# Kernel tuning notes

Hardware: AMD Instinct MI355X
Metric: run time of the kernel (lower is better)

## Reference

```python
import jax, jax.numpy as jnp
import numpy as np

D_IN = 1024
D_OUT = 1024

def setup_inputs() -> dict:
    key = jax.random.key(0)
    kx, kq, kk, kv = jax.random.split(key, 4)
    x = jax.random.normal(kx, (4, 4096, D_IN), dtype=jnp.float32)
    s = 1.0 / np.sqrt(D_IN)
    Wq = jax.random.uniform(kq, (D_IN, D_OUT), dtype=jnp.float32, minval=-s, maxval=s)
    Wk = jax.random.uniform(kk, (D_IN, D_OUT), dtype=jnp.float32, minval=-s, maxval=s)
    Wv = jax.random.uniform(kv, (D_IN, D_OUT), dtype=jnp.float32, minval=-s, maxval=s)
    return {"x": x, "Wq": Wq, "Wk": Wk, "Wv": Wv}

def reference(x, Wq, Wk, Wv):
    # x: [B, S, d_in]; single-head causal attention (dropout p=0 => identity)
    B, S, _ = x.shape
    Q = jnp.einsum('bsd,de->bse', x, Wq)
    K = jnp.einsum('bsd,de->bse', x, Wk)
    V = jnp.einsum('bsd,de->bse', x, Wv)
    scale = 1.0 / jnp.sqrt(jnp.asarray(K.shape[-1], dtype=Q.dtype))
    scores = jnp.einsum('bqe,bke->bqk', Q, K) * scale  # [B, S, S]
    causal = jnp.tril(jnp.ones((S, S), dtype=bool))     # mask upper triangle (diag=1)
    scores = jnp.where(causal, scores, -jnp.inf)
    weights = jax.nn.softmax(scores, axis=-1)
    return jnp.einsum('bqk,bke->bqe', weights, V)
```

## Files before the change

### kernel.cpp

```cpp
#include <hip/hip_runtime.h>
#include <hip/hip_bf16.h>
#include <stdint.h>

typedef short short8 __attribute__((ext_vector_type(8)));
typedef short short4v __attribute__((ext_vector_type(4)));
typedef float f32x4 __attribute__((ext_vector_type(4)));

static __device__ __forceinline__ short f2bf(float f) {
  union { float f; uint32_t u; } v; v.f = f;
  uint32_t r = (v.u + 0x7fffu + ((v.u >> 16) & 1u)) >> 16;
  return (short)(uint16_t)r;
}
static __device__ __forceinline__ float bf2f(short h) {
  union { uint32_t u; float f; } v; v.u = ((uint32_t)(uint16_t)h) << 16;
  return v.f;
}

#define MFMA(a, b, c) __builtin_amdgcn_mfma_f32_16x16x32_bf16((a), (b), (c), 0, 0, 0)

static __device__ __forceinline__ void gload16(const short* g, short* l) {
  __builtin_amdgcn_global_load_lds(
      (const __attribute__((address_space(1))) void*)g,
      (__attribute__((address_space(3))) void*)l, 16, 0, 0);
}

static __device__ __forceinline__ void gemm256_m201(
    const short* __restrict__ Ag, int lda,
    const short* __restrict__ Bg, int ldb, int kext,
    short* lds, int t, f32x4 (&acc)[8][4])
{
  const int w = t >> 6, lane = t & 63;
  const int lr = lane & 15, lk = lane >> 4;
  const int wm = w >> 2, wn = w & 3;
  const int nk = kext >> 6;

  short* const Ab0 = lds;
  short* const Ab1 = lds + 16384;
  short* const Bb0 = lds + 32768;
  short* const Bb1 = lds + 49152;

  const int qr = t >> 3;
  const int qc = (t & 7) ^ (qr & 7);
  const short* Asrc = Ag + (size_t)qr * lda + qc * 8;
  const short* Bsrc = Bg + (size_t)qr * ldb + qc * 8;

#define STAGE_A(tile, q) gload16(Asrc + (size_t)(q) * 64 * lda + (tile) * 64, \
    (((tile) & 1) ? Ab1 : Ab0) + (q) * 4096 + w * 512)
#define STAGE_B(tile, q) gload16(Bsrc + (size_t)(q) * 64 * ldb + (tile) * 64, \
    (((tile) & 1) ? Bb1 : Bb0) + (q) * 4096 + w * 512)

  const int chq0 = ((lk) ^ (lr & 7)) * 8;
  const int chq1 = ((4 + lk) ^ (lr & 7)) * 8;
  const int arow0 = (wm * 128 + lr) * 64;
  const int brow0 = (wn * 64 + lr) * 64;

  STAGE_B(0, 0); STAGE_B(0, 2); STAGE_B(0, 1); STAGE_B(0, 3);
  STAGE_A(0, 0); STAGE_A(0, 2); STAGE_A(0, 1); STAGE_A(0, 3);
  asm volatile("s_waitcnt vmcnt(2)" ::: "memory");
  __builtin_amdgcn_s_barrier();

  for (int tt = 0; tt < nk; ++tt) {
    const short* Ac = (tt & 1) ? Ab1 : Ab0;
    const short* Bc = (tt & 1) ? Bb1 : Bb0;
    const int nx = tt + 1;
    const bool st = nx < nk;
    short8 b0[4], b1[4], af[4];

#pragma unroll
    for (int mt = 0; mt < 4; ++mt)
      af[mt] = *(const short8*)&Ac[arow0 + mt * 1024 + chq0];
#pragma unroll
    for (int nt = 0; nt < 4; ++nt)
      b0[nt] = *(const short8*)&Bc[brow0 + nt * 1024 + chq0];
    if (st) { STAGE_B(nx, 0); STAGE_B(nx, 2); }
    __builtin_amdgcn_s_barrier();
    asm volatile("s_waitcnt lgkmcnt(0)" ::: "memory");
    __builtin_amdgcn_sched_barrier(0);
    __builtin_amdgcn_s_setprio(1);
#pragma unroll
    for (int mt = 0; mt < 4; ++mt)
#pragma unroll
      for (int nt = 0; nt < 4; ++nt)
        acc[mt][nt] = MFMA(af[mt], b0[nt], acc[mt][nt]);
    __builtin_amdgcn_s_setprio(0);
    __builtin_amdgcn_s_barrier();

#pragma unroll
    for (int mt = 0; mt < 4; ++mt)
      af[mt] = *(const short8*)&Ac[arow0 + mt * 1024 + chq1];
#pragma unroll
    for (int nt = 0; nt < 4; ++nt)
      b1[nt] = *(const short8*)&Bc[brow0 + nt * 1024 + chq1];
    if (st) { STAGE_B(nx, 1); STAGE_B(nx, 3); }
    __builtin_amdgcn_s_barrier();
    asm volatile("s_waitcnt lgkmcnt(0)" ::: "memory");
    __builtin_amdgcn_sched_barrier(0);
    __builtin_amdgcn_s_setprio(1);
#pragma unroll
    for (int mt = 0; mt < 4; ++mt)
#pragma unroll
      for (int nt = 0; nt < 4; ++nt)
        acc[mt][nt] = MFMA(af[mt], b1[nt], acc[mt][nt]);
    __builtin_amdgcn_s_setprio(0);
    if (st) { asm volatile("s_waitcnt vmcnt(4)" ::: "memory"); }
    else    { asm volatile("s_waitcnt vmcnt(0)" ::: "memory"); }
    __builtin_amdgcn_s_barrier();

#pragma unroll
    for (int mt = 0; mt < 4; ++mt)
      af[mt] = *(const short8*)&Ac[arow0 + 4096 + mt * 1024 + chq0];
    if (st) { STAGE_A(nx, 0); STAGE_A(nx, 2); }
    __builtin_amdgcn_s_barrier();
    asm volatile("s_waitcnt lgkmcnt(0)" ::: "memory");
    __builtin_amdgcn_sched_barrier(0);
    __builtin_amdgcn_s_setprio(1);
#pragma unroll
    for (int mt = 0; mt < 4; ++mt)
#pragma unroll
      for (int nt = 0; nt < 4; ++nt)
        acc[4 + mt][nt] = MFMA(af[mt], b0[nt], acc[4 + mt][nt]);
    __builtin_amdgcn_s_setprio(0);
    __builtin_amdgcn_s_barrier();

#pragma unroll
    for (int mt = 0; mt < 4; ++mt)
      af[mt] = *(const short8*)&Ac[arow0 + 4096 + mt * 1024 + chq1];
    if (st) { STAGE_A(nx, 1); STAGE_A(nx, 3); }
    __builtin_amdgcn_s_barrier();
    asm volatile("s_waitcnt lgkmcnt(0)" ::: "memory");
    __builtin_amdgcn_sched_barrier(0);
    __builtin_amdgcn_s_setprio(1);
#pragma unroll
    for (int mt = 0; mt < 4; ++mt)
#pragma unroll
      for (int nt = 0; nt < 4; ++nt)
        acc[4 + mt][nt] = MFMA(af[mt], b1[nt], acc[4 + mt][nt]);
    __builtin_amdgcn_s_setprio(0);
    if (st) { asm volatile("s_waitcnt vmcnt(2)" ::: "memory"); }
    else    { asm volatile("s_waitcnt vmcnt(0)" ::: "memory"); }
    __builtin_amdgcn_s_barrier();
  }
#undef STAGE_A
#undef STAGE_B
}

static __device__ __forceinline__ void gemm_tile128(
    const short* __restrict__ Ag, int lda,
    const short* __restrict__ Bg, int ldb, int kext,
    short* Alds, short* Blds, int w, int lane, f32x4 (&acc)[4][4])
{
  const int wr = (w >> 1) * 64, wc = (w & 1) * 64;
  const int lr = lane & 15, lk = lane >> 4;

  const int c0 = w * 128 + lane;
  const int c1 = c0 + 64;
  const int r0 = c0 >> 2, cg0 = (c0 & 3) ^ ((r0 >> 1) & 3);
  const int r1 = c1 >> 2, cg1 = (c1 & 3) ^ ((r1 >> 1) & 3);
  const short* a0 = Ag + (size_t)r0 * lda + cg0 * 8;
  const short* a1 = Ag + (size_t)r1 * lda + cg1 * 8;
  const short* b0 = Bg + (size_t)r0 * ldb + cg0 * 8;
  const short* b1 = Bg + (size_t)r1 * ldb + cg1 * 8;
  short* la0 = Alds + w * 1024;
  short* la1 = la0 + 512;
  short* lb0 = Blds + w * 1024;
  short* lb1 = lb0 + 512;

  int ra[4], rb[4];
#pragma unroll
  for (int mt = 0; mt < 4; ++mt) {
    int rl = wr + mt * 16 + lr;
    ra[mt] = rl * 32 + (lk ^ ((rl >> 1) & 3)) * 8;
  }
#pragma unroll
  for (int nt = 0; nt < 4; ++nt) {
    int rl = wc + nt * 16 + lr;
    rb[nt] = rl * 32 + (lk ^ ((rl >> 1) & 3)) * 8;
  }

  for (int kk = 0; kk < kext; kk += 32) {
    if (kk) __syncthreads();
    gload16(a0 + kk, la0);
    gload16(a1 + kk, la1);
    gload16(b0 + kk, lb0);
    gload16(b1 + kk, lb1);
    __syncthreads();
    short8 af[4], bfr[4];
#pragma unroll
    for (int mt = 0; mt < 4; ++mt) af[mt] = *(const short8*)&Alds[ra[mt]];
#pragma unroll
    for (int nt = 0; nt < 4; ++nt) bfr[nt] = *(const short8*)&Blds[rb[nt]];
#pragma unroll
    for (int mt = 0; mt < 4; ++mt)
#pragma unroll
      for (int nt = 0; nt < 4; ++nt)
        acc[mt][nt] = MFMA(af[mt], bfr[nt], acc[mt][nt]);
  }
}

__global__ __launch_bounds__(256)
void cvt_x(const float* __restrict__ x, short* __restrict__ xb) {
  size_t i = (size_t)blockIdx.x * 256 + threadIdx.x;
  f32x4 a = *(const f32x4*)(x + i * 8);
  f32x4 b = *(const f32x4*)(x + i * 8 + 4);
  short8 h = { f2bf(a.x), f2bf(a.y), f2bf(a.z), f2bf(a.w),
               f2bf(b.x), f2bf(b.y), f2bf(b.z), f2bf(b.w) };
  *(short8*)(xb + i * 8) = h;
}

__global__ __launch_bounds__(256)
void cvt_w(const float* __restrict__ Wq, const float* __restrict__ Wk,
           const float* __restrict__ Wv, short* __restrict__ wt) {
  __shared__ short Tl[128][136];
  const int z = blockIdx.z;
  const float* W = (z == 0) ? Wq : (z == 1) ? Wk : Wv;
  const float scale = (z == 0) ? 0.03125f : 1.0f;
  const int c0 = blockIdx.x * 128, r0 = blockIdx.y * 128;
  const int t = threadIdx.x;
#pragma unroll
  for (int j = 0; j < 16; ++j) {
    int id = j * 256 + t;
    int row = id >> 5, c4 = id & 31;
    f32x4 v = *(const f32x4*)(W + (size_t)(r0 + row) * 1024 + c0 + c4 * 4);
#pragma unroll
    for (int cc = 0; cc < 4; ++cc) Tl[c4 * 4 + cc][row] = f2bf(v[cc] * scale);
  }
  __syncthreads();
  short* dst = wt + (size_t)z * 1048576;
#pragma unroll
  for (int j = 0; j < 8; ++j) {
    int id = j * 256 + t;
    int col = id >> 4, r8 = id & 15;
    *(short8*)(dst + (size_t)(c0 + col) * 1024 + r0 + r8 * 8) =
        *(const short8*)&Tl[col][r8 * 8];
  }
}

__global__ __launch_bounds__(512, 2)
void qkv_gemm(const short* __restrict__ xb, const short* __restrict__ wt,
              short* __restrict__ q, short* __restrict__ k,
              short* __restrict__ vt) {
  extern __shared__ short lds[];
  const int z = blockIdx.z;
  const int n0 = blockIdx.x * 256, m0 = blockIdx.y * 256;
  const int t = threadIdx.x;
  f32x4 acc[8][4] = {};
  gemm256_m201(xb + (size_t)m0 * 1024, 1024,
               wt + (size_t)z * 1048576 + (size_t)n0 * 1024, 1024, 1024,
               lds, t, acc);
  const int w = t >> 6, lane = t & 63;
  const int lr = lane & 15, lk = lane >> 4;
  const int wm = w >> 2, wn = w & 3;
#pragma unroll
  for (int mt = 0; mt < 8; ++mt) {
#pragma unroll
    for (int nt = 0; nt < 4; ++nt) {
      int col = n0 + wn * 64 + nt * 16 + lr;
      int rbase = m0 + wm * 128 + mt * 16 + lk * 4;
      if (z == 2) {
        int bb = rbase >> 12, s = rbase & 4095;
        short4v h = { f2bf(acc[mt][nt][0]), f2bf(acc[mt][nt][1]),
                      f2bf(acc[mt][nt][2]), f2bf(acc[mt][nt][3]) };
        *(short4v*)(vt + ((size_t)bb * 1024 + col) * 4096 + s) = h;
      } else {
        short* dst = (z == 0) ? q : k;
#pragma unroll
        for (int i = 0; i < 4; ++i)
          dst[(size_t)(rbase + i) * 1024 + col] = f2bf(acc[mt][nt][i]);
      }
    }
  }
}

__global__ __launch_bounds__(512, 2)
void s_gemm(const short* __restrict__ q, const short* __restrict__ k,
            short* __restrict__ P, float* __restrict__ lpart) {
  extern __shared__ short lds[];
  const int bid = blockIdx.x;
  const int b = bid & 3, tt = bid >> 2;
  int ti = (int)((sqrtf(8.f * tt + 1.f) - 1.f) * 0.5f);
  while ((ti + 1) * (ti + 2) / 2 <= tt) ++ti;
  while (ti * (ti + 1) / 2 > tt) --ti;
  const int tj = tt - ti * (ti + 1) / 2;
  const int t = threadIdx.x;
  f32x4 acc[8][4] = {};
  gemm256_m201(q + ((size_t)(b * 4096 + ti * 256)) * 1024, 1024,
               k + ((size_t)(b * 4096 + tj * 256)) * 1024, 1024, 1024,
               lds, t, acc);
  const int w = t >> 6, lane = t & 63;
  const int lr = lane & 15, lk = lane >> 4;
  const int wm = w >> 2, wn = w & 3;
  const bool diag = (ti == tj);
#pragma unroll
  for (int mt = 0; mt < 8; ++mt) {
#pragma unroll
    for (int i = 0; i < 4; ++i) {
      const int rl = wm * 128 + mt * 16 + lk * 4 + i;
      size_t prow = ((size_t)(b * 4096 + ti * 256 + rl)) * 4096 + tj * 256;
      float rs = 0.f;
#pragma unroll
      for (int nt = 0; nt < 4; ++nt) {
        const int cl = wn * 64 + nt * 16 + lr;
        float e = (!diag || cl <= rl) ? __expf(acc[mt][nt][i]) : 0.f;
        short pb = f2bf(e);
        P[prow + cl] = pb;
        rs += bf2f(pb);
      }
      rs += __shfl_xor(rs, 1);
      rs += __shfl_xor(rs, 2);
      rs += __shfl_xor(rs, 4);
      rs += __shfl_xor(rs, 8);
      if (lr == 0)
        lpart[((size_t)(tj * 4 + wn)) * 16384 + b * 4096 + ti * 256 + rl] = rs;
    }
  }
}

__global__ __launch_bounds__(256)
void l_reduce(const float* __restrict__ lpart, float* __restrict__ lsum) {
  int idx = blockIdx.x * 256 + threadIdx.x;
  int qq = idx & 4095;
  int ti = qq >> 8;
  float s = 0.f;
  for (int tj = 0; tj <= ti; ++tj) {
#pragma unroll
    for (int e = 0; e < 4; ++e)
      s += lpart[(size_t)(tj * 4 + e) * 16384 + idx];
  }
  lsum[idx] = s;
}

__global__ __launch_bounds__(256)
void pv_gemm(const short* __restrict__ P, const short* __restrict__ vt,
             const float* __restrict__ lsum, float* __restrict__ out) {
  __shared__ short Alds[128 * 32], Blds[128 * 32];
  const int bid = blockIdx.x;
  const int b = bid & 3;
  const int r = bid >> 2;
  const int dt = r & 7;
  const int qt = 31 - (r >> 3);
  const int t = threadIdx.x, w = t >> 6, lane = t & 63;
  f32x4 acc[4][4] = {};
  gemm_tile128(P + ((size_t)(b * 4096 + qt * 128)) * 4096, 4096,
               vt + ((size_t)(b * 1024 + dt * 128)) * 4096, 4096,
               (qt + 1) * 128, Alds, Blds, w, lane, acc);
  const int lr = lane & 15, lk = lane >> 4;
  const int wr = (w >> 1) * 64, wc = (w & 1) * 64;
#pragma unroll
  for (int mt = 0; mt < 4; ++mt) {
#pragma unroll
    for (int i = 0; i < 4; ++i) {
      int rl = wr + mt * 16 + lk * 4 + i;
      int grow = b * 4096 + qt * 128 + rl;
      float inv = 1.0f / lsum[grow];
#pragma unroll
      for (int nt = 0; nt < 4; ++nt) {
        int cl = wc + nt * 16 + lr;
        out[(size_t)grow * 1024 + dt * 128 + cl] = acc[mt][nt][i] * inv;
      }
    }
  }
}

extern "C" void kernel_launch(void* const* d_in, const int* in_sizes, int n_in,
                              void* d_out, int out_size, void* d_ws, size_t ws_size,
                              hipStream_t stream) {
  (void)in_sizes; (void)n_in; (void)out_size; (void)ws_size;
  const float* x  = (const float*)d_in[0];
  const float* Wq = (const float*)d_in[1];
  const float* Wk = (const float*)d_in[2];
  const float* Wv = (const float*)d_in[3];
  float* out = (float*)d_out;

  short* q_ws  = (short*)d_ws;
  short* k_ws  = q_ws + (size_t)16777216;
  short* vt_ws = k_ws + (size_t)16777216;
  short* P     = vt_ws + (size_t)16777216;
  short* xb    = P;
  float* lpart = (float*)(P + (size_t)67108864);
  float* lsum  = lpart + (size_t)64 * 16384;
  short* wt    = (short*)(lsum + 16384);

  const int gemm_lds = 131072;
  hipFuncSetAttribute((const void*)qkv_gemm,
                      hipFuncAttributeMaxDynamicSharedMemorySize, gemm_lds);
  hipFuncSetAttribute((const void*)s_gemm,
                      hipFuncAttributeMaxDynamicSharedMemorySize, gemm_lds);

  cvt_x<<<dim3(8192), 256, 0, stream>>>(x, xb);
  cvt_w<<<dim3(8, 8, 3), 256, 0, stream>>>(Wq, Wk, Wv, wt);
  qkv_gemm<<<dim3(4, 64, 3), 512, gemm_lds, stream>>>(xb, wt, q_ws, k_ws, vt_ws);
  s_gemm<<<dim3(544), 512, gemm_lds, stream>>>(q_ws, k_ws, P, lpart);
  l_reduce<<<dim3(64), 256, 0, stream>>>(lpart, lsum);
  pv_gemm<<<dim3(1024), 256, 0, stream>>>(P, vt_ws, lsum, out);
}
```

Before: 339.3 us.

## Fuse Q/K/V projections into one 128-tile GEMM sharing the A tile

Replaces the 256x256 QKV projection kernel, which launched one block per output matrix, with a 128x128-tile kernel that computes Q, K and V together. Each block loads one x tile and reuses it against three weight tiles per k-step, so x is read from memory once instead of three times. The new kernel uses static 32 KB LDS, 256 threads and single-buffered k-steps of 32 with a sync on every step, which loses the double-buffered pipelining of the old GEMM. It also holds 192 accumulator registers per thread, which may limit occupancy.

```diff
diff --git a/kernel.cpp b/kernel.cpp
--- a/kernel.cpp
+++ b/kernel.cpp
@@ -22,6 +22,67 @@
   __builtin_amdgcn_global_load_lds(
       (const __attribute__((address_space(1))) void*)g,
       (__attribute__((address_space(3))) void*)l, 16, 0, 0);
+}
+
+static __device__ __forceinline__ void gemm_tile128_z3(
+    const short* __restrict__ Ag, int lda,
+    const short* __restrict__ Bg0, const short* __restrict__ Bg1,
+    const short* __restrict__ Bg2, int ldb, int kext,
+    short* Alds, short* Blds, int w, int lane, f32x4 (&acc)[3][4][4])
+{
+  const int wr = (w >> 1) * 64, wc = (w & 1) * 64;
+  const int lr = lane & 15, lk = lane >> 4;
+
+  const int c0 = w * 128 + lane;
+  const int c1 = c0 + 64;
+  const int r0 = c0 >> 2, cg0 = (c0 & 3) ^ ((r0 >> 1) & 3);
+  const int r1 = c1 >> 2, cg1 = (c1 & 3) ^ ((r1 >> 1) & 3);
+  const short* a0 = Ag + (size_t)r0 * lda + cg0 * 8;
+  const short* a1 = Ag + (size_t)r1 * lda + cg1 * 8;
+  const size_t bo0 = (size_t)r0 * ldb + cg0 * 8;
+  const size_t bo1 = (size_t)r1 * ldb + cg1 * 8;
+  short* la0 = Alds + w * 1024;
+  short* la1 = la0 + 512;
+
+  int ra[4], rb[4];
+#pragma unroll
+  for (int mt = 0; mt < 4; ++mt) {
+    int rl = wr + mt * 16 + lr;
+    ra[mt] = rl * 32 + (lk ^ ((rl >> 1) & 3)) * 8;
+  }
+#pragma unroll
+  for (int nt = 0; nt < 4; ++nt) {
+    int rl = wc + nt * 16 + lr;
+    rb[nt] = rl * 32 + (lk ^ ((rl >> 1) & 3)) * 8;
+  }
+
+  for (int kk = 0; kk < kext; kk += 32) {
+    if (kk) __syncthreads();
+    gload16(a0 + kk, la0);
+    gload16(a1 + kk, la1);
+    gload16(Bg0 + bo0 + kk, Blds + w * 1024);
+    gload16(Bg0 + bo1 + kk, Blds + w * 1024 + 512);
+    gload16(Bg1 + bo0 + kk, Blds + 4096 + w * 1024);
+    gload16(Bg1 + bo1 + kk, Blds + 4096 + w * 1024 + 512);
+    gload16(Bg2 + bo0 + kk, Blds + 8192 + w * 1024);
+    gload16(Bg2 + bo1 + kk, Blds + 8192 + w * 1024 + 512);
+    __syncthreads();
+    short8 af[4];
+#pragma unroll
+    for (int mt = 0; mt < 4; ++mt) af[mt] = *(const short8*)&Alds[ra[mt]];
+#pragma unroll
+    for (int z = 0; z < 3; ++z) {
+      short8 bfr[4];
+#pragma unroll
+      for (int nt = 0; nt < 4; ++nt)
+        bfr[nt] = *(const short8*)&Blds[z * 4096 + rb[nt]];
+#pragma unroll
+      for (int mt = 0; mt < 4; ++mt)
+#pragma unroll
+        for (int nt = 0; nt < 4; ++nt)
+          acc[z][mt][nt] = MFMA(af[mt], bfr[nt], acc[z][mt][nt]);
+    }
+  }
 }
 
 static __device__ __forceinline__ void gemm256_m201(
@@ -235,37 +296,41 @@
   }
 }
 
-__global__ __launch_bounds__(512, 2)
+__global__ __launch_bounds__(256)
 void qkv_gemm(const short* __restrict__ xb, const short* __restrict__ wt,
               short* __restrict__ q, short* __restrict__ k,
               short* __restrict__ vt) {
-  extern __shared__ short lds[];
-  const int z = blockIdx.z;
-  const int n0 = blockIdx.x * 256, m0 = blockIdx.y * 256;
-  const int t = threadIdx.x;
-  f32x4 acc[8][4] = {};
-  gemm256_m201(xb + (size_t)m0 * 1024, 1024,
-               wt + (size_t)z * 1048576 + (size_t)n0 * 1024, 1024, 1024,
-               lds, t, acc);
-  const int w = t >> 6, lane = t & 63;
-  const int lr = lane & 15, lk = lane >> 4;
-  const int wm = w >> 2, wn = w & 3;
-#pragma unroll
-  for (int mt = 0; mt < 8; ++mt) {
-#pragma unroll
-    for (int nt = 0; nt < 4; ++nt) {
-      int col = n0 + wn * 64 + nt * 16 + lr;
-      int rbase = m0 + wm * 128 + mt * 16 + lk * 4;
-      if (z == 2) {
-        int bb = rbase >> 12, s = rbase & 4095;
-        short4v h = { f2bf(acc[mt][nt][0]), f2bf(acc[mt][nt][1]),
-                      f2bf(acc[mt][nt][2]), f2bf(acc[mt][nt][3]) };
-        *(short4v*)(vt + ((size_t)bb * 1024 + col) * 4096 + s) = h;
-      } else {
-        short* dst = (z == 0) ? q : k;
-#pragma unroll
-        for (int i = 0; i < 4; ++i)
-          dst[(size_t)(rbase + i) * 1024 + col] = f2bf(acc[mt][nt][i]);
+  __shared__ short Alds[128 * 32];
+  __shared__ short Blds[3 * 128 * 32];
+  const int n0 = blockIdx.x * 128, m0 = blockIdx.y * 128;
+  const int t = threadIdx.x, w = t >> 6, lane = t & 63;
+  f32x4 acc[3][4][4] = {};
+  gemm_tile128_z3(xb + (size_t)m0 * 1024, 1024,
+                  wt + (size_t)n0 * 1024,
+                  wt + 1048576 + (size_t)n0 * 1024,
+                  wt + 2097152 + (size_t)n0 * 1024, 1024, 1024,
+                  Alds, Blds, w, lane, acc);
+  const int lr = lane & 15, lk = lane >> 4;
+  const int wr = (w >> 1) * 64, wc = (w & 1) * 64;
+#pragma unroll
+  for (int z = 0; z < 3; ++z) {
+#pragma unroll
+    for (int mt = 0; mt < 4; ++mt) {
+#pragma unroll
+      for (int nt = 0; nt < 4; ++nt) {
+        int col = n0 + wc + nt * 16 + lr;
+        int rbase = m0 + wr + mt * 16 + lk * 4;
+        if (z == 2) {
+          int bb = rbase >> 12, s = rbase & 4095;
+          short4v h = { f2bf(acc[2][mt][nt][0]), f2bf(acc[2][mt][nt][1]),
+                        f2bf(acc[2][mt][nt][2]), f2bf(acc[2][mt][nt][3]) };
+          *(short4v*)(vt + ((size_t)bb * 1024 + col) * 4096 + s) = h;
+        } else {
+          short* dst = (z == 0) ? q : k;
+#pragma unroll
+          for (int i = 0; i < 4; ++i)
+            dst[(size_t)(rbase + i) * 1024 + col] = f2bf(acc[z][mt][nt][i]);
+        }
       }
     }
   }
@@ -381,14 +446,12 @@
   short* wt    = (short*)(lsum + 16384);
 
   const int gemm_lds = 131072;
-  hipFuncSetAttribute((const void*)qkv_gemm,
-                      hipFuncAttributeMaxDynamicSharedMemorySize, gemm_lds);
   hipFuncSetAttribute((const void*)s_gemm,
                       hipFuncAttributeMaxDynamicSharedMemorySize, gemm_lds);
 
   cvt_x<<<dim3(8192), 256, 0, stream>>>(x, xb);
   cvt_w<<<dim3(8, 8, 3), 256, 0, stream>>>(Wq, Wk, Wv, wt);
-  qkv_gemm<<<dim3(4, 64, 3), 512, gemm_lds, stream>>>(xb, wt, q_ws, k_ws, vt_ws);
+  qkv_gemm<<<dim3(8, 128), 256, 0, stream>>>(xb, wt, q_ws, k_ws, vt_ws);
   s_gemm<<<dim3(544), 512, gemm_lds, stream>>>(q_ws, k_ws, P, lpart);
   l_reduce<<<dim3(64), 256, 0, stream>>>(lpart, lsum);
   pv_gemm<<<dim3(1024), 256, 0, stream>>>(P, vt_ws, lsum, out);
```

New measurement: 406.9 us. 19.9% more time.
